# Optimization experiments

Measured on AMD Instinct MI355X. Metric: run time of the kernel, lower is better.

## Reference

```python
import jax, jax.numpy as jnp
from jax import lax
import numpy as np

N = 2000            # number of RPN proposals
NUM_CLASSES = 21    # Pascal-VOC classes (incl. background, as the original loops all classes)
MAX_PER_CLASS = 50
MAX_PER_IMAGE = 100
IOU_THR = 0.7
NEG = jnp.float32(-1e9)


def setup_inputs() -> dict:
    key = jax.random.key(0)
    k1, k2, k3, k4 = jax.random.split(key, 4)
    # valid [y1, x1, y2, x2] proposals inside a ~600x600 image
    yx = jax.random.uniform(k1, (N, 2), dtype=jnp.float32) * 600.0
    hw = jax.random.uniform(k2, (N, 2), dtype=jnp.float32) * 120.0 + 16.0
    rpn_proposals_bboxes = jnp.concatenate([yx, yx + hw], axis=1)
    roi_bboxes_txtytwth = jax.random.normal(k3, (N, 4), dtype=jnp.float32) * 0.1
    roi_score = jax.random.uniform(k4, (N, NUM_CLASSES), dtype=jnp.float32)
    return {
        "rpn_proposals_bboxes": rpn_proposals_bboxes,
        "roi_bboxes_txtytwth": roi_bboxes_txtytwth,
        "roi_score": roi_score,
    }


def _decode_bbox(props, deltas):
    h = props[:, 2] - props[:, 0]
    w = props[:, 3] - props[:, 1]
    cy = props[:, 0] + 0.5 * h
    cx = props[:, 1] + 0.5 * w
    dy, dx, dh, dw = deltas[:, 0], deltas[:, 1], deltas[:, 2], deltas[:, 3]
    pcy = dy * h + cy
    pcx = dx * w + cx
    ph = h * jnp.exp(dh)
    pw = w * jnp.exp(dw)
    return jnp.stack([pcy - 0.5 * ph, pcx - 0.5 * pw, pcy + 0.5 * ph, pcx + 0.5 * pw], axis=1)


def _pairwise_iou(boxes):
    # boxes: [N,4] -> iou [N,N]
    y1, x1, y2, x2 = boxes[:, 0], boxes[:, 1], boxes[:, 2], boxes[:, 3]
    area = (y2 - y1) * (x2 - x1)                      # [N]
    iy1 = jnp.maximum(y1[:, None], y1[None, :])
    ix1 = jnp.maximum(x1[:, None], x1[None, :])
    iy2 = jnp.minimum(y2[:, None], y2[None, :])
    ix2 = jnp.minimum(x2[:, None], x2[None, :])
    inter = jnp.maximum(iy2 - iy1, 0.0) * jnp.maximum(ix2 - ix1, 0.0)
    union = area[:, None] + area[None, :] - inter
    return inter / jnp.maximum(union, 1e-8)


def _nms_keep(iou_sorted):
    # iou_sorted: [N,N] IoU among boxes already sorted by descending score.
    # Greedy NMS: box i kept iff no earlier kept box overlaps it > IOU_THR.
    def body(kept, xs):
        row, i = xs                                    # row: iou of box i vs all
        suppressed = jnp.any(kept & (row > IOU_THR))
        kept = kept.at[i].set(~suppressed)
        return kept, None
    kept, _ = lax.scan(body, jnp.zeros((N,), dtype=bool), (iou_sorted, jnp.arange(N)))
    return kept


def reference(rpn_proposals_bboxes, roi_bboxes_txtytwth, roi_score):
    final_bboxes = _decode_bbox(rpn_proposals_bboxes, roi_bboxes_txtytwth)   # [N,4]
    iou = _pairwise_iou(final_bboxes)                                        # [N,N]

    # per-class descending score order
    order = jnp.argsort(-roi_score.T, axis=1)                                # [C,N]
    scores_sorted = jnp.take_along_axis(roi_score.T, order, axis=1)          # [C,N]
    # reorder IoU per class: [C,N,N]
    iou_sorted = jax.vmap(lambda o: iou[o][:, o])(order)
    kept = jax.vmap(_nms_keep)(iou_sorted)                                   # [C,N] bool
    # cap at MAX_PER_CLASS kept boxes per class (NMS max_output_size)
    rank = jnp.cumsum(kept.astype(jnp.int32), axis=1)
    valid = kept & (rank <= MAX_PER_CLASS)
    masked_scores = jnp.where(valid, scores_sorted, NEG)                     # [C,N]

    boxes_sorted = final_bboxes[order]                                       # [C,N,4]
    cls_ids = jnp.broadcast_to(jnp.arange(NUM_CLASSES, dtype=jnp.int32)[:, None], (NUM_CLASSES, N))

    # global top-k over all surviving (class, box) pairs
    flat_scores = masked_scores.reshape(-1)                                  # [C*N]
    _, idx = lax.top_k(flat_scores, MAX_PER_IMAGE)
    out_bboxes = boxes_sorted.reshape(-1, 4)[idx]                            # [K,4]
    out_cls = cls_ids.reshape(-1)[idx]                                       # [K]
    return out_bboxes, out_cls
```

## Files before the change

### kernel.cpp

```cpp
#include <hip/hip_runtime.h>

#define N 2000
#define NCLS 21
#define MAXPC 50
#define MAXPI 100
#define IOU_THR 0.7f

typedef unsigned long long u64;
typedef unsigned int u32;

__device__ __forceinline__ u32 sortable(float s) {
    u32 u = __float_as_uint(s);
    return ((int)u < 0) ? ~u : (u | 0x80000000u);
}

__device__ __forceinline__ float4 decode_one(const float* __restrict__ rpn,
                                             const float* __restrict__ deltas, int i) {
    float4 p = ((const float4*)rpn)[i];
    float4 d = ((const float4*)deltas)[i];
    float h = p.z - p.x, w = p.w - p.y;
    float cy = p.x + 0.5f * h, cx = p.y + 0.5f * w;
    float pcy = d.x * h + cy;
    float pcx = d.y * w + cx;
    float ph = h * expf(d.z);
    float pw = w * expf(d.w);
    return make_float4(pcy - 0.5f * ph, pcx - 0.5f * pw, pcy + 0.5f * ph, pcx + 0.5f * pw);
}

__device__ __forceinline__ float iou_vs(float4 b, float ar,
                                        float kx, float ky, float kz, float kw) {
    float ka = (kz - kx) * (kw - ky);
    float iy1 = fmaxf(b.x, kx), ix1 = fmaxf(b.y, ky);
    float iy2 = fminf(b.z, kz), ix2 = fminf(b.w, kw);
    float inter = fmaxf(iy2 - iy1, 0.f) * fmaxf(ix2 - ix1, 0.f);
    return inter / fmaxf(ar + ka - inter, 1e-8f);
}

__global__ void sort_kernel(const float* __restrict__ score, int* __restrict__ order) {
    __shared__ __align__(16) u64 skey[N];
    int c = blockIdx.x;
    for (int i = threadIdx.x; i < N; i += blockDim.x) {
        u32 u = sortable(score[i * NCLS + c]);
        skey[i] = ((u64)u << 32) | (u32)(~i);
    }
    __syncthreads();
    int i = blockIdx.y * 64 + (threadIdx.x >> 2);
    int q = threadIdx.x & 3;
    if (i < N) {
        u64 ki = skey[i];
        const ulonglong2* s2 = (const ulonglong2*)skey;
        int r = 0;
        int jj0 = q * 250;
#pragma unroll 4
        for (int jj = jj0; jj < jj0 + 250; jj++) {
            ulonglong2 v = s2[jj];
            r += (v.x > ki);
            r += (v.y > ki);
        }
        r += __shfl_xor(r, 1);
        r += __shfl_xor(r, 2);
        if (q == 0) order[c * N + r] = i;
    }
}

__global__ void __launch_bounds__(1024, 1)
nms_topk_kernel(const float* __restrict__ rpn, const float* __restrict__ deltas,
                const float* __restrict__ score,
                const int* __restrict__ order,
                int* __restrict__ keep_pos, int* __restrict__ keep_cnt,
                u64* __restrict__ cand_key,
                u32* __restrict__ done,
                float* __restrict__ out) {
    __shared__ __align__(16) float4 sbox[N];
    __shared__ u32 skey[N];
    __shared__ float4 kbox[MAXPC];
    __shared__ u64 tk[NCLS * MAXPC];
    __shared__ int scnt[NCLS];
    __shared__ int s_flag;

    int c = blockIdx.x;
    int tid = threadIdx.x;

    for (int pos = tid; pos < N; pos += 1024) {
        int oi = order[c * N + pos];
        sbox[pos] = decode_one(rpn, deltas, oi);
        skey[pos] = sortable(score[oi * NCLS + c]);
    }
    __syncthreads();

    if (tid < 64) {
        int lane = tid;
        int nk = 0;
        const int NCH = (N + 63) / 64;
        for (int chunk = 0; chunk < NCH && nk < MAXPC; chunk++) {
            int pos = chunk * 64 + lane;
            bool valid = pos < N;
            float4 bb = sbox[valid ? pos : (N - 1)];
            float ar = (bb.z - bb.x) * (bb.w - bb.y);
            bool sup = !valid;
            for (int k = 0; k < nk; k++) {
                float4 kb = kbox[k];
                sup = sup || (iou_vs(bb, ar, kb.x, kb.y, kb.z, kb.w) > IOU_THR);
            }
            u64 alive = __ballot(!sup);
            while (alive && nk < MAXPC) {
                int l = __ffsll((unsigned long long)alive) - 1;
                if (lane == l) {
                    kbox[nk] = bb;
                    keep_pos[c * MAXPC + nk] = pos;
                    cand_key[c * MAXPC + nk] =
                        ((u64)skey[pos] << 32) | (u32)(~(c * N + pos));
                }
                float4 nbx = kbox[nk];
                nk++;
                if (lane > l && !sup)
                    sup = (iou_vs(bb, ar, nbx.x, nbx.y, nbx.z, nbx.w) > IOU_THR);
                u64 nb = __ballot(!sup);
                alive = (l >= 63) ? 0ull : (nb & (~0ull << (l + 1)));
            }
        }
        if (lane == 0) keep_cnt[c] = nk;
    }
    __syncthreads();

    if (tid == 0) {
        u32 old = __hip_atomic_fetch_add(done, 1u, __ATOMIC_RELEASE,
                                         __HIP_MEMORY_SCOPE_AGENT);
        s_flag = ((old % 21u) == 20u);
    }
    __syncthreads();
    if (!s_flag) return;
    __builtin_amdgcn_fence(__ATOMIC_ACQUIRE, "agent");

    for (int t = tid; t < NCLS * MAXPC; t += 1024)
        tk[t] = cand_key[t];
    if (tid < NCLS) scnt[tid] = keep_cnt[tid];
    __syncthreads();
    int M = 0;
#pragma unroll
    for (int c2 = 0; c2 < NCLS; c2++) M += scnt[c2];

    for (int t = tid; t < NCLS * MAXPC; t += 1024) {
        int cc = t / MAXPC, k = t - cc * MAXPC;
        if (k >= scnt[cc]) continue;
        u64 ki = tk[t];
        int r = k;
#pragma unroll
        for (int c2 = 0; c2 < NCLS; c2++) {
            if (c2 == cc) continue;
            int lo = 0, hi = scnt[c2];
            while (lo < hi) {
                int mid = (lo + hi) >> 1;
                if (tk[c2 * MAXPC + mid] > ki) lo = mid + 1; else hi = mid;
            }
            r += lo;
        }
        if (r < MAXPI) {
            int flat = (int)(~(u32)ki);
            int pos = flat - cc * N;
            int oi = order[cc * N + pos];
            float4 bb = decode_one(rpn, deltas, oi);
            out[r * 4 + 0] = bb.x;
            out[r * 4 + 1] = bb.y;
            out[r * 4 + 2] = bb.z;
            out[r * 4 + 3] = bb.w;
            out[4 * MAXPI + r] = (float)cc;
        }
    }
    if (tid == 0 && M < MAXPI) {
        int m = M;
        int cnt0 = scnt[0];
        for (int pos = 0; pos < 150 && m < MAXPI; pos++) {
            bool validp = false;
            for (int k = 0; k < cnt0; k++)
                if (keep_pos[k] == pos) { validp = true; break; }
            if (!validp) {
                int oi = order[pos];
                float4 bb = decode_one(rpn, deltas, oi);
                out[m * 4 + 0] = bb.x;
                out[m * 4 + 1] = bb.y;
                out[m * 4 + 2] = bb.z;
                out[m * 4 + 3] = bb.w;
                out[4 * MAXPI + m] = 0.0f;
                m++;
            }
        }
    }
}

extern "C" void kernel_launch(void* const* d_in, const int* in_sizes, int n_in,
                              void* d_out, int out_size, void* d_ws, size_t ws_size,
                              hipStream_t stream) {
    const float* rpn    = (const float*)d_in[0];
    const float* deltas = (const float*)d_in[1];
    const float* score  = (const float*)d_in[2];
    float* out = (float*)d_out;

    char* ws = (char*)d_ws;
    int*   order    = (int*)(ws);
    u64*   candk    = (u64*)(ws + 168000);
    int*   keep_pos = (int*)(ws + 176400);
    int*   keep_cnt = (int*)(ws + 180600);
    u32*   done     = (u32*)(ws + 180736);

    sort_kernel<<<dim3(NCLS, 32), 256, 0, stream>>>(score, order);
    nms_topk_kernel<<<NCLS, 1024, 0, stream>>>(rpn, deltas, score, order,
                                               keep_pos, keep_cnt, candk, done, out);
}
```

Measured before the change: 54.58 us.

## Split NMS and top-k into separate kernels with lazy chunk decode and bitmask NMS

The fused NMS+top-k kernel is split into a single-wavefront-per-class NMS kernel and a one-block top-k kernel, which removes the atomic last-block-done handoff. NMS now decodes boxes one 64-wide chunk at a time instead of decoding all 2000 up front into LDS, so early exit after 50 keeps skips most of the decode work. Within a chunk, a 64x64 suppression bitmask is precomputed and the serial keep loop uses ballots over that mask rather than recomputing IoU per kept box. The cost is an extra kernel launch and a fixed 64-step ballot loop per chunk.

```diff
diff --git a/kernel.cpp b/kernel.cpp
--- a/kernel.cpp
+++ b/kernel.cpp
@@ -63,75 +63,64 @@
     }
 }
 
-__global__ void __launch_bounds__(1024, 1)
-nms_topk_kernel(const float* __restrict__ rpn, const float* __restrict__ deltas,
-                const float* __restrict__ score,
-                const int* __restrict__ order,
-                int* __restrict__ keep_pos, int* __restrict__ keep_cnt,
-                u64* __restrict__ cand_key,
-                u32* __restrict__ done,
-                float* __restrict__ out) {
-    __shared__ __align__(16) float4 sbox[N];
-    __shared__ u32 skey[N];
+__global__ void nms_kernel(const float* __restrict__ rpn,
+                           const float* __restrict__ deltas,
+                           const int* __restrict__ order,
+                           const float* __restrict__ score,
+                           int* __restrict__ keep_pos,
+                           int* __restrict__ keep_cnt,
+                           u64* __restrict__ cand_key) {
+    __shared__ float4 cbox[64];
     __shared__ float4 kbox[MAXPC];
-    __shared__ u64 tk[NCLS * MAXPC];
-    __shared__ int scnt[NCLS];
-    __shared__ int s_flag;
-
     int c = blockIdx.x;
-    int tid = threadIdx.x;
-
-    for (int pos = tid; pos < N; pos += 1024) {
-        int oi = order[c * N + pos];
-        sbox[pos] = decode_one(rpn, deltas, oi);
-        skey[pos] = sortable(score[oi * NCLS + c]);
-    }
-    __syncthreads();
-
-    if (tid < 64) {
-        int lane = tid;
-        int nk = 0;
-        const int NCH = (N + 63) / 64;
-        for (int chunk = 0; chunk < NCH && nk < MAXPC; chunk++) {
-            int pos = chunk * 64 + lane;
-            bool valid = pos < N;
-            float4 bb = sbox[valid ? pos : (N - 1)];
-            float ar = (bb.z - bb.x) * (bb.w - bb.y);
-            bool sup = !valid;
-            for (int k = 0; k < nk; k++) {
-                float4 kb = kbox[k];
-                sup = sup || (iou_vs(bb, ar, kb.x, kb.y, kb.z, kb.w) > IOU_THR);
-            }
-            u64 alive = __ballot(!sup);
-            while (alive && nk < MAXPC) {
-                int l = __ffsll((unsigned long long)alive) - 1;
+    int lane = threadIdx.x;
+    int nk = 0;
+    const int NCH = (N + 63) / 64;
+    for (int chunk = 0; chunk < NCH && nk < MAXPC; chunk++) {
+        int pos = chunk * 64 + lane;
+        bool valid = pos < N;
+        int oi = order[c * N + (valid ? pos : (N - 1))];
+        float4 bb = decode_one(rpn, deltas, oi);
+        cbox[lane] = bb;
+        float ar = (bb.z - bb.x) * (bb.w - bb.y);
+        bool sup = !valid;
+        for (int k = 0; k < nk; k++) {
+            float4 kb = kbox[k];
+            sup = sup || (iou_vs(bb, ar, kb.x, kb.y, kb.z, kb.w) > IOU_THR);
+        }
+        u64 supby = 0;
+#pragma unroll 4
+        for (int j = 0; j < 64; j++) {
+            float4 bj = cbox[j];
+            supby |= (u64)(iou_vs(bb, ar, bj.x, bj.y, bj.z, bj.w) > IOU_THR) << j;
+        }
+        u64 alive = __ballot(!sup);
+        for (int l = 0; l < 64 && nk < MAXPC; l++) {
+            u64 col = __ballot((supby >> l) & 1);
+            if ((alive >> l) & 1) {
                 if (lane == l) {
                     kbox[nk] = bb;
                     keep_pos[c * MAXPC + nk] = pos;
-                    cand_key[c * MAXPC + nk] =
-                        ((u64)skey[pos] << 32) | (u32)(~(c * N + pos));
+                    u32 u = sortable(score[oi * NCLS + c]);
+                    cand_key[c * MAXPC + nk] = ((u64)u << 32) | (u32)(~(c * N + pos));
                 }
-                float4 nbx = kbox[nk];
                 nk++;
-                if (lane > l && !sup)
-                    sup = (iou_vs(bb, ar, nbx.x, nbx.y, nbx.z, nbx.w) > IOU_THR);
-                u64 nb = __ballot(!sup);
-                alive = (l >= 63) ? 0ull : (nb & (~0ull << (l + 1)));
+                alive &= ~(col & (~0ull << (l + 1)));
             }
         }
-        if (lane == 0) keep_cnt[c] = nk;
     }
-    __syncthreads();
+    if (lane == 0) keep_cnt[c] = nk;
+}
 
-    if (tid == 0) {
-        u32 old = __hip_atomic_fetch_add(done, 1u, __ATOMIC_RELEASE,
-                                         __HIP_MEMORY_SCOPE_AGENT);
-        s_flag = ((old % 21u) == 20u);
-    }
-    __syncthreads();
-    if (!s_flag) return;
-    __builtin_amdgcn_fence(__ATOMIC_ACQUIRE, "agent");
-
+__global__ void __launch_bounds__(1024, 1)
+topk_kernel(const float* __restrict__ rpn, const float* __restrict__ deltas,
+            const int* __restrict__ order,
+            const int* __restrict__ keep_pos, const int* __restrict__ keep_cnt,
+            const u64* __restrict__ cand_key,
+            float* __restrict__ out) {
+    __shared__ u64 tk[NCLS * MAXPC];
+    __shared__ int scnt[NCLS];
+    int tid = threadIdx.x;
     for (int t = tid; t < NCLS * MAXPC; t += 1024)
         tk[t] = cand_key[t];
     if (tid < NCLS) scnt[tid] = keep_cnt[tid];
@@ -201,9 +190,10 @@
     u64*   candk    = (u64*)(ws + 168000);
     int*   keep_pos = (int*)(ws + 176400);
     int*   keep_cnt = (int*)(ws + 180600);
-    u32*   done     = (u32*)(ws + 180736);
 
     sort_kernel<<<dim3(NCLS, 32), 256, 0, stream>>>(score, order);
-    nms_topk_kernel<<<NCLS, 1024, 0, stream>>>(rpn, deltas, score, order,
-                                               keep_pos, keep_cnt, candk, done, out);
+    nms_kernel<<<NCLS, 64, 0, stream>>>(rpn, deltas, order, score,
+                                        keep_pos, keep_cnt, candk);
+    topk_kernel<<<1, 1024, 0, stream>>>(rpn, deltas, order,
+                                        keep_pos, keep_cnt, candk, out);
 }
```

New measurement: 53.76 us. No clear change (-1.5%).
